# Kernel tuning notes

Hardware: AMD Instinct MI355X
Metric: run time of the kernel (lower is better)

Reference implementation:

```python
import jax, jax.numpy as jnp
import numpy as np


def setup_inputs() -> dict:
    key = jax.random.key(0)
    ks = jax.random.split(key, 8)
    B, S, V, E, H = 64, 128, 8000, 256, 512
    scale = 0.05
    return {
        "inputs": jax.random.randint(ks[0], (B, S), 0, V, dtype=jnp.int64),
        "embedding": jax.random.normal(ks[1], (V, E), dtype=jnp.float32) * scale,
        "W_ih": jax.random.normal(ks[2], (4 * H, E), dtype=jnp.float32) * scale,
        "W_hh": jax.random.normal(ks[3], (4 * H, H), dtype=jnp.float32) * scale,
        "b_ih": jax.random.normal(ks[4], (4 * H,), dtype=jnp.float32) * scale,
        "b_hh": jax.random.normal(ks[5], (4 * H,), dtype=jnp.float32) * scale,
        "W_cls": jax.random.normal(ks[6], (V, H), dtype=jnp.float32) * scale,
        "b_cls": jax.random.normal(ks[7], (V,), dtype=jnp.float32) * scale,
    }


def reference(inputs, embedding, W_ih, W_hh, b_ih, b_hh, W_cls, b_cls):
    B, S = inputs.shape
    H = W_hh.shape[1]
    x = embedding[inputs]  # (B, S, E)
    # batch the input-to-hidden GEMM across all timesteps
    x_gates = jnp.einsum('bse,ge->bsg', x, W_ih) + b_ih + b_hh  # (B, S, 4H)

    def step(carry, xg):
        h, c = carry
        gates = xg + h @ W_hh.T  # (B, 4H)
        i, f, g, o = jnp.split(gates, 4, axis=-1)  # PyTorch LSTMCell gate order
        i = jax.nn.sigmoid(i)
        f = jax.nn.sigmoid(f)
        g = jnp.tanh(g)
        o = jax.nn.sigmoid(o)
        c = f * c + i * g
        h = o * jnp.tanh(c)
        return (h, c), h

    h0 = jnp.zeros((B, H), dtype=x.dtype)
    c0 = jnp.zeros((B, H), dtype=x.dtype)
    _, hs = jax.lax.scan(step, (h0, c0), jnp.swapaxes(x_gates, 0, 1))  # hs: (S, B, H)
    hidden = jnp.swapaxes(hs, 0, 1)  # (B, S, H)
    logits = jnp.einsum('bsh,vh->bsv', hidden, W_cls) + b_cls  # (B, S, V)
    y = jnp.transpose(logits, (0, 2, 1))  # (B, V, S)
    return jax.nn.log_softmax(y, axis=1)
```

## Files before the change

### kernel.cpp

```cpp
#include <hip/hip_runtime.h>


using u16   = unsigned short;
using u32   = unsigned int;
using u16x8 = __attribute__((ext_vector_type(8))) u16;
using bf16x8 = __attribute__((ext_vector_type(8))) __bf16;
using f32x4 = __attribute__((ext_vector_type(4))) float;

#define NB   64
#define NS   128
#define NV   8000
#define NVP  8192
#define NE   256
#define NH   512
#define NG   2048
#define NBS  8192
#define OUT_BSTRIDE 1024000
#define XG_SSTRIDE  131072

__device__ inline u16 f2bf(float f) {
    unsigned x = __builtin_bit_cast(unsigned, f);
    unsigned r = (x + 0x7FFFu + ((x >> 16) & 1u)) >> 16;
    return (u16)r;
}

__device__ inline bf16x8 ld_frag(const u16* p) {
    u16x8 v = *(const u16x8*)p;
    return __builtin_bit_cast(bf16x8, v);
}

__device__ inline u32 load_llc(const u32* p) {
    u32 v;
    asm volatile("global_load_dword %0, %1, off sc0 sc1\n\t"
                 "s_waitcnt vmcnt(0)"
                 : "=v"(v) : "v"(p) : "memory");
    return v;
}
__device__ inline f32x4 load_llc16(const void* p) {
    f32x4 v;
    asm volatile("global_load_dwordx4 %0, %1, off sc0 sc1\n\t"
                 "s_waitcnt vmcnt(0)"
                 : "=v"(v) : "v"(p) : "memory");
    return v;
}
__device__ inline void store_llc(u32* p, u32 v) {
    asm volatile("global_store_dword %0, %1, off sc0 sc1"
                 :: "v"(p), "v"(v) : "memory");
}
__device__ inline void prefetch16(f32x4& d, const float* p) {
    asm volatile("global_load_dwordx4 %0, %1, off"
                 : "=v"(d) : "v"(p) : "memory");
}

__device__ inline void quad_transpose(float v[4], int p) {
    float tb[4];
    #pragma unroll
    for (int q2 = 0; q2 < 4; ++q2) tb[q2] = __shfl_xor(v[q2 ^ 2], 2);
    #pragma unroll
    for (int q2 = 0; q2 < 4; ++q2) v[q2] = (((q2 ^ p) & 2) ? tb[q2] : v[q2]);
    #pragma unroll
    for (int q2 = 0; q2 < 4; ++q2) tb[q2] = __shfl_xor(v[q2 ^ 1], 1);
    #pragma unroll
    for (int q2 = 0; q2 < 4; ++q2) v[q2] = (((q2 ^ p) & 1) ? tb[q2] : v[q2]);
}

__device__ inline float lstm_cell(const float v[4], float& c) {
    float i_ = 1.f / (1.f + __expf(-v[0]));
    float f_ = 1.f / (1.f + __expf(-v[1]));
    float e2 = __expf(2.f * v[2]);
    float g_ = 1.f - 2.f / (e2 + 1.f);
    float o_ = 1.f / (1.f + __expf(-v[3]));
    c = f_ * c + i_ * g_;
    float e2c = __expf(2.f * c);
    return o_ * (1.f - 2.f / (e2c + 1.f));
}

__global__ void cvt_bf16(const float* __restrict__ s, u16* __restrict__ d, int n8) {
    const float4* s4 = (const float4*)s;
    for (int i = blockIdx.x * blockDim.x + threadIdx.x; i < n8;
         i += gridDim.x * blockDim.x) {
        float4 a = s4[2 * i], b = s4[2 * i + 1];
        u16x8 o;
        o[0] = f2bf(a.x); o[1] = f2bf(a.y); o[2] = f2bf(a.z); o[3] = f2bf(a.w);
        o[4] = f2bf(b.x); o[5] = f2bf(b.y); o[6] = f2bf(b.z); o[7] = f2bf(b.w);
        ((u16x8*)d)[i] = o;
    }
}

__global__ __launch_bounds__(256) void k1_xgates(
    const u16* __restrict__ Wih, const u16* __restrict__ emb,
    const int* __restrict__ toks,
    const float* __restrict__ bih, const float* __restrict__ bhh,
    float* __restrict__ xg)
{
    __shared__ u16x8 Al8[512];
    __shared__ u16x8 Bl8[512];
    u16* Al = (u16*)Al8;
    u16* Bl = (u16*)Bl8;

    const int t = threadIdx.x;
    const int lane = t & 63, w = t >> 6;
    const int wm = w >> 1, wn = w & 1;
    const int gtile = blockIdx.y * 128, mtile = blockIdx.x * 128;

    const int r0 = t >> 2, r1 = r0 + 64, q = t & 3;
    const int m0 = mtile + r0, m1 = mtile + r1;
    const int tok0 = toks[(m0 & 63) * NS + (m0 >> 6)];
    const int tok1 = toks[(m1 & 63) * NS + (m1 >> 6)];

    f32x4 acc[4][4];
    for (int i = 0; i < 4; ++i)
        for (int j = 0; j < 4; ++j) acc[i][j] = {0.f, 0.f, 0.f, 0.f};

    const int kc8 = (lane >> 4) * 8;
    for (int kk = 0; kk < 8; ++kk) {
        const int k0 = kk * 32;
        *(u16x8*)&Al[t * 8]         = *(const u16x8*)&Wih[(gtile + r0) * NE + k0 + q * 8];
        *(u16x8*)&Al[(t + 256) * 8] = *(const u16x8*)&Wih[(gtile + r1) * NE + k0 + q * 8];
        *(u16x8*)&Bl[t * 8]         = *(const u16x8*)&emb[tok0 * NE + k0 + q * 8];
        *(u16x8*)&Bl[(t + 256) * 8] = *(const u16x8*)&emb[tok1 * NE + k0 + q * 8];
        __syncthreads();
        bf16x8 af[4], bf[4];
        #pragma unroll
        for (int i = 0; i < 4; ++i) {
            af[i] = ld_frag(&Al[(wm * 64 + i * 16 + (lane & 15)) * 32 + kc8]);
            bf[i] = ld_frag(&Bl[(wn * 64 + i * 16 + (lane & 15)) * 32 + kc8]);
        }
        #pragma unroll
        for (int fi = 0; fi < 4; ++fi)
            #pragma unroll
            for (int fj = 0; fj < 4; ++fj)
                acc[fi][fj] = __builtin_amdgcn_mfma_f32_16x16x32_bf16(
                    af[fi], bf[fj], acc[fi][fj], 0, 0, 0);
        __syncthreads();
    }

    #pragma unroll
    for (int fi = 0; fi < 4; ++fi) {
        const int g0 = gtile + wm * 64 + fi * 16 + ((lane >> 4) << 2);
        const float4 v1 = *(const float4*)&bih[g0];
        const float4 v2 = *(const float4*)&bhh[g0];
        float badd[4] = {v1.x + v2.x, v1.y + v2.y, v1.z + v2.z, v1.w + v2.w};
        #pragma unroll
        for (int fj = 0; fj < 4; ++fj) {
            const int m = mtile + wn * 64 + fj * 16 + (lane & 15);
            const int b = m & 63, s = m >> 6;
            float* dst = &xg[s * XG_SSTRIDE + b];
            #pragma unroll
            for (int r = 0; r < 4; ++r)
                dst[(g0 + r) * 64] = acc[fi][fj][r] + badd[r];
        }
    }
}

#define LSTM_NBLK 64

__global__ __launch_bounds__(512, 2) void k2_lstm(
    const u16* __restrict__ Whh,
    const float* __restrict__ xg,
    u16* __restrict__ hbuf,
    u16* __restrict__ hidden,
    u32* __restrict__ flags)
{
    __shared__ __align__(16) u16 hl[16 * 528];

    const int t = threadIdx.x, lane = t & 63, w = t >> 6;
    const int bg = blockIdx.x >> 3, ug = blockIdx.x & 7;
    const int j = lane & 15, kg = lane >> 4;
    const int kc8 = kg * 8;

    const int ubase = ug * 64 + w * 8;
    const int grow0 = (j & 3) * 512 + ubase + (j >> 2);
    const int grow1 = grow0 + 4;

    bf16x8 bw0[16], bw1[16];
    #pragma unroll
    for (int kk = 0; kk < 16; ++kk) {
        bw0[kk] = ld_frag(&Whh[grow0 * NH + kk * 32 + kc8]);
        bw1[kk] = ld_frag(&Whh[grow1 * NH + kk * 32 + kc8]);
    }
    #pragma unroll
    for (int kk = 0; kk < 16; ++kk) {
        f32x4 w0 = __builtin_bit_cast(f32x4, bw0[kk]);
        f32x4 w1 = __builtin_bit_cast(f32x4, bw1[kk]);
        asm volatile("" : "+v"(w0), "+v"(w1));
        bw0[kk] = __builtin_bit_cast(bf16x8, w0);
        bw1[kk] = __builtin_bit_cast(bf16x8, w1);
    }

    {
        u16x8 z = {0, 0, 0, 0, 0, 0, 0, 0};
        *(u16x8*)&hl[(8 + (t >> 6)) * 528 + (t & 63) * 8] = z;
    }

    const int srow = t >> 6, scol = (t & 63) * 8;
    const int soff = (bg * 8 + srow) * NH + scol;
    u16* hl_w = &hl[srow * 528 + scol];

    const int p  = lane & 3;
    const int q  = (lane >> 2) & 3;
    const int mb = kg * 4;
    const bool real = (kg < 2);
    const int bat = bg * 8 + mb + p;
    const int un0 = ubase + q;
    const bool sl = real && ((lane & 4) == 0);

    const int xo0 = grow0 * 64 + bg * 8 + mb;
    const int xo1 = grow1 * 64 + bg * 8 + mb;

    f32x4 xvA0 = {0,0,0,0}, xvA1 = {0,0,0,0};
    f32x4 xvB0 = {0,0,0,0}, xvB1 = {0,0,0,0};
    if (real) {
        xvA0 = *(const f32x4*)&xg[xo0];
        xvA1 = *(const f32x4*)&xg[xo1];
        xvB0 = *(const f32x4*)&xg[XG_SSTRIDE + xo0];
        xvB1 = *(const f32x4*)&xg[XG_SSTRIDE + xo1];
    }
    float cA = 0.f, cB = 0.f;

    auto body = [&](int step, f32x4& X0, f32x4& X1) {
        f32x4 a00 = {0,0,0,0}, a01 = {0,0,0,0};
        f32x4 a10 = {0,0,0,0}, a11 = {0,0,0,0};

        if (step > 0) {
            if (lane < 8) {
                const u32* fp = &flags[(bg * 8 + lane) * 32];
                while ((int)load_llc(fp) < step) __builtin_amdgcn_s_sleep(1);
            }
            f32x4 hv = load_llc16(&hbuf[(step & 1) * (NB * NH) + soff]);
            *(f32x4*)hl_w = hv;
            __syncthreads();

            #pragma unroll
            for (int kk = 0; kk < 16; ++kk) {
                bf16x8 av = *(const bf16x8*)&hl[j * 528 + kk * 32 + kc8];
                if (kk & 1) {
                    a01 = __builtin_amdgcn_mfma_f32_16x16x32_bf16(av, bw0[kk], a01, 0, 0, 0);
                    a11 = __builtin_amdgcn_mfma_f32_16x16x32_bf16(av, bw1[kk], a11, 0, 0, 0);
                } else {
                    a00 = __builtin_amdgcn_mfma_f32_16x16x32_bf16(av, bw0[kk], a00, 0, 0, 0);
                    a10 = __builtin_amdgcn_mfma_f32_16x16x32_bf16(av, bw1[kk], a10, 0, 0, 0);
                }
            }
        }

        float v0[4], v1[4];
        #pragma unroll
        for (int r = 0; r < 4; ++r) {
            v0[r] = a00[r] + a01[r] + X0[r];
            v1[r] = a10[r] + a11[r] + X1[r];
        }
        quad_transpose(v0, p);
        quad_transpose(v1, p);

        float h0 = lstm_cell(v0, cA);
        float h1 = lstm_cell(v1, cB);
        u32 hb0 = f2bf(h0), hb1 = f2bf(h1);
        u32 o0 = (u32)__shfl_xor((int)hb0, 4);
        u32 o1 = (u32)__shfl_xor((int)hb1, 4);
        u32 pr0 = hb0 | (o0 << 16);
        u32 pr1 = hb1 | (o1 << 16);

        if (step + 1 < NS && sl) {
            u32* hp = (u32*)&hbuf[((step + 1) & 1) * (NB * NH) + bat * NH + un0];
            store_llc(hp, pr0);
            store_llc(hp + 2, pr1);
        }
        if (step + 2 < NS && real) {
            const float* xb = &xg[(step + 2) * XG_SSTRIDE];
            prefetch16(X0, &xb[xo0]);
            prefetch16(X1, &xb[xo1]);
        }
        if (step + 2 < NS)
            asm volatile("s_waitcnt vmcnt(2) lgkmcnt(0)\n\ts_barrier" ::: "memory");
        else
            asm volatile("s_waitcnt vmcnt(0) lgkmcnt(0)\n\ts_barrier" ::: "memory");
        if (step + 1 < NS && t == 0)
            store_llc(&flags[blockIdx.x * 32], (u32)(step + 1));
        if (sl) {
            *(u32*)&hidden[(bat * NS + step) * NH + un0] = pr0;
            *(u32*)&hidden[(bat * NS + step) * NH + un0 + 4] = pr1;
        }
    };

    for (int s2 = 0; s2 < NS / 2; ++s2) {
        body(2 * s2,     xvA0, xvA1);
        body(2 * s2 + 1, xvB0, xvB1);
    }
}

__global__ __launch_bounds__(256) void k3_cls(
    const u16* __restrict__ Wc, const u16* __restrict__ hid,
    const float* __restrict__ bcls,
    float* __restrict__ out, float* __restrict__ lse)
{
    __shared__ u16x8 Al8[512];
    __shared__ u16x8 Bl8[512];
    __shared__ float red[2][128];
    u16* Al = (u16*)Al8;
    u16* Bl = (u16*)Bl8;

    const int t = threadIdx.x;
    const int lane = t & 63, w = t >> 6;
    const int wm = w >> 1, wn = w & 1;
    const int vtile = blockIdx.y * 128, mtile = blockIdx.x * 128;

    const int r0 = t >> 2, r1 = r0 + 64, q = t & 3;

    f32x4 acc[4][4];
    for (int i = 0; i < 4; ++i)
        for (int j2 = 0; j2 < 4; ++j2) acc[i][j2] = {0.f, 0.f, 0.f, 0.f};

    const int kc8 = (lane >> 4) * 8;
    for (int kk = 0; kk < 16; ++kk) {
        const int k0 = kk * 32;
        *(u16x8*)&Al[t * 8]         = *(const u16x8*)&Wc[(vtile + r0) * NH + k0 + q * 8];
        *(u16x8*)&Al[(t + 256) * 8] = *(const u16x8*)&Wc[(vtile + r1) * NH + k0 + q * 8];
        *(u16x8*)&Bl[t * 8]         = *(const u16x8*)&hid[(mtile + r0) * NH + k0 + q * 8];
        *(u16x8*)&Bl[(t + 256) * 8] = *(const u16x8*)&hid[(mtile + r1) * NH + k0 + q * 8];
        __syncthreads();
        bf16x8 af[4], bf[4];
        #pragma unroll
        for (int i = 0; i < 4; ++i) {
            af[i] = ld_frag(&Al[(wm * 64 + i * 16 + (lane & 15)) * 32 + kc8]);
            bf[i] = ld_frag(&Bl[(wn * 64 + i * 16 + (lane & 15)) * 32 + kc8]);
        }
        #pragma unroll
        for (int fi = 0; fi < 4; ++fi)
            #pragma unroll
            for (int fj = 0; fj < 4; ++fj)
                acc[fi][fj] = __builtin_amdgcn_mfma_f32_16x16x32_bf16(
                    af[fi], bf[fj], acc[fi][fj], 0, 0, 0);
        __syncthreads();
    }

    float lsum[4] = {0.f, 0.f, 0.f, 0.f};
    #pragma unroll
    for (int fi = 0; fi < 4; ++fi) {
        const int v0 = vtile + wm * 64 + fi * 16 + ((lane >> 4) << 2);
        const bool vok = (v0 < NV);
        float4 bc = {0.f, 0.f, 0.f, 0.f};
        if (vok) bc = *(const float4*)&bcls[v0];
        #pragma unroll
        for (int fj = 0; fj < 4; ++fj) {
            const int m = mtile + wn * 64 + fj * 16 + (lane & 15);
            const int b = m >> 7, s = m & 127;
            if (vok) {
                float* dst = &out[b * OUT_BSTRIDE + v0 * NS + s];
                float e = 0.f;
                #pragma unroll
                for (int r = 0; r < 4; ++r) {
                    float lg = acc[fi][fj][r] + (&bc.x)[r];
                    dst[r * NS] = lg;
                    e += __expf(lg);
                }
                lsum[fj] += e;
            }
        }
    }
    #pragma unroll
    for (int fj = 0; fj < 4; ++fj) {
        lsum[fj] += __shfl_xor(lsum[fj], 16);
        lsum[fj] += __shfl_xor(lsum[fj], 32);
    }
    if (lane < 16) {
        #pragma unroll
        for (int fj = 0; fj < 4; ++fj)
            red[wm][wn * 64 + fj * 16 + lane] = lsum[fj];
    }
    __syncthreads();
    if (t < 128) {
        const int m = mtile + t;
        atomicAdd(&lse[m], red[0][t] + red[1][t]);
    }
}

__global__ void k4_log(const float* __restrict__ lse, float* __restrict__ ll) {
    int i = blockIdx.x * 256 + threadIdx.x;
    if (i < NBS) ll[i] = logf(lse[i]);
}

__global__ void k5_norm(float* __restrict__ out, const float* __restrict__ ll) {
    const int total4 = NB * NV * NS / 4;
    float4* o4 = (float4*)out;
    for (int i = blockIdx.x * blockDim.x + threadIdx.x; i < total4;
         i += gridDim.x * blockDim.x) {
        const int i4 = i * 4;
        const int b = i4 / OUT_BSTRIDE;
        const int s = (i4 - b * OUT_BSTRIDE) & 127;
        float4 v = o4[i];
        const float4 l = *(const float4*)&ll[b * NS + s];
        v.x -= l.x; v.y -= l.y; v.z -= l.z; v.w -= l.w;
        o4[i] = v;
    }
}

extern "C" void kernel_launch(void* const* d_in, const int* in_sizes, int n_in,
                              void* d_out, int out_size, void* d_ws, size_t ws_size,
                              hipStream_t stream) {
    const int*   toks   = (const int*)d_in[0];
    const float* emb_f  = (const float*)d_in[1];
    const float* Wih_f  = (const float*)d_in[2];
    const float* Whh_f  = (const float*)d_in[3];
    const float* bih    = (const float*)d_in[4];
    const float* bhh    = (const float*)d_in[5];
    const float* Wcls_f = (const float*)d_in[6];
    const float* bcls   = (const float*)d_in[7];
    float* out = (float*)d_out;
    char*  ws  = (char*)d_ws;

    u32*   flags  = (u32*)(ws + 0);
    float* lse    = (float*)(ws + 8192);
    float* loglse = (float*)(ws + 40960);
    u16*   hbuf   = (u16*)(ws + 73728);
    u16*   embb   = (u16*)(ws + 204800);
    u16*   wihb   = (u16*)(ws + 4300800);
    u16*   whhb   = (u16*)(ws + 5349376);
    u16*   wclsb  = (u16*)(ws + 7446528);
    u16*   hidden = (u16*)(ws + 15835136);

    float* xg = out;

    hipMemsetAsync(ws, 0, 73728, stream);
    hipMemsetAsync((char*)wclsb + NV * NH * 2, 0, (NVP - NV) * NH * 2, stream);

    cvt_bf16<<<1024, 256, 0, stream>>>(emb_f,  embb,  NV * NE / 8);
    cvt_bf16<<<256,  256, 0, stream>>>(Wih_f,  wihb,  NG * NE / 8);
    cvt_bf16<<<512,  256, 0, stream>>>(Whh_f,  whhb,  NG * NH / 8);
    cvt_bf16<<<1024, 256, 0, stream>>>(Wcls_f, wclsb, NV * NH / 8);

    k1_xgates<<<dim3(64, 16), 256, 0, stream>>>(wihb, embb, toks, bih, bhh, xg);
    k2_lstm<<<LSTM_NBLK, 512, 0, stream>>>(whhb, xg, hbuf, hidden, flags);
    k3_cls<<<dim3(64, 64), 256, 0, stream>>>(wclsb, hidden, bcls, out, lse);
    k4_log<<<32, 256, 0, stream>>>(lse, loglse);
    k5_norm<<<2048, 256, 0, stream>>>(out, loglse);
}
```

Before: 684.3 us.

## Use per-wave flags and double-buffered LDS to drop the second block barrier per LSTM step

Replaces the per-block completion flag with one flag per wave, posted after that wave's hidden-state stores drain. Each thread now spins on a single producer-wave flag instead of eight lanes polling block flags. The shared h tile is double-buffered by step parity, so only one __syncthreads per step is needed and the trailing barrier is removed. The xg prefetch distance drops from two steps to one. The cost is more flag traffic and polling spread across all lanes, and the correctness of the flag indexing has to hold across blocks.

```diff
diff --git a/kernel.cpp b/kernel.cpp
--- a/kernel.cpp
+++ b/kernel.cpp
@@ -162,7 +162,7 @@
     u16* __restrict__ hidden,
     u32* __restrict__ flags)
 {
-    __shared__ __align__(16) u16 hl[16 * 528];
+    __shared__ __align__(16) u16 hl[2][16 * 528];
 
     const int t = threadIdx.x, lane = t & 63, w = t >> 6;
     const int bg = blockIdx.x >> 3, ug = blockIdx.x & 7;
@@ -190,12 +190,14 @@
 
     {
         u16x8 z = {0, 0, 0, 0, 0, 0, 0, 0};
-        *(u16x8*)&hl[(8 + (t >> 6)) * 528 + (t & 63) * 8] = z;
+        *(u16x8*)&hl[0][(8 + (t >> 6)) * 528 + (t & 63) * 8] = z;
+        *(u16x8*)&hl[1][(8 + (t >> 6)) * 528 + (t & 63) * 8] = z;
     }
 
     const int srow = t >> 6, scol = (t & 63) * 8;
     const int soff = (bg * 8 + srow) * NH + scol;
-    u16* hl_w = &hl[srow * 528 + scol];
+    const u32* myflag = flags + bg * 256 + (t & 63) * 4;
+    u32* ourflag = flags + bg * 256 + (ug * 8 + w) * 4;
 
     const int p  = lane & 3;
     const int q  = (lane >> 2) & 3;
@@ -208,32 +210,35 @@
     const int xo0 = grow0 * 64 + bg * 8 + mb;
     const int xo1 = grow1 * 64 + bg * 8 + mb;
 
-    f32x4 xvA0 = {0,0,0,0}, xvA1 = {0,0,0,0};
-    f32x4 xvB0 = {0,0,0,0}, xvB1 = {0,0,0,0};
+    f32x4 xv0 = {0,0,0,0}, xv1 = {0,0,0,0};
+    f32x4 xn0 = {0,0,0,0}, xn1 = {0,0,0,0};
     if (real) {
-        xvA0 = *(const f32x4*)&xg[xo0];
-        xvA1 = *(const f32x4*)&xg[xo1];
-        xvB0 = *(const f32x4*)&xg[XG_SSTRIDE + xo0];
-        xvB1 = *(const f32x4*)&xg[XG_SSTRIDE + xo1];
+        xv0 = *(const f32x4*)&xg[xo0];
+        xv1 = *(const f32x4*)&xg[xo1];
     }
     float cA = 0.f, cB = 0.f;
 
-    auto body = [&](int step, f32x4& X0, f32x4& X1) {
+    for (int step = 0; step < NS; ++step) {
+        const int par = step & 1;
+        if (step > 0) {
+            while ((int)load_llc(myflag) < step) __builtin_amdgcn_s_sleep(1);
+            f32x4 hv = load_llc16(&hbuf[par * (NB * NH) + soff]);
+            *(f32x4*)&hl[par][srow * 528 + scol] = hv;
+        }
+        __syncthreads();
+
+        if (step + 1 < NS && real) {
+            const float* xb = &xg[(step + 1) * XG_SSTRIDE];
+            prefetch16(xn0, &xb[xo0]);
+            prefetch16(xn1, &xb[xo1]);
+        }
+
         f32x4 a00 = {0,0,0,0}, a01 = {0,0,0,0};
         f32x4 a10 = {0,0,0,0}, a11 = {0,0,0,0};
-
         if (step > 0) {
-            if (lane < 8) {
-                const u32* fp = &flags[(bg * 8 + lane) * 32];
-                while ((int)load_llc(fp) < step) __builtin_amdgcn_s_sleep(1);
-            }
-            f32x4 hv = load_llc16(&hbuf[(step & 1) * (NB * NH) + soff]);
-            *(f32x4*)hl_w = hv;
-            __syncthreads();
-
             #pragma unroll
             for (int kk = 0; kk < 16; ++kk) {
-                bf16x8 av = *(const bf16x8*)&hl[j * 528 + kk * 32 + kc8];
+                bf16x8 av = *(const bf16x8*)&hl[par][j * 528 + kk * 32 + kc8];
                 if (kk & 1) {
                     a01 = __builtin_amdgcn_mfma_f32_16x16x32_bf16(av, bw0[kk], a01, 0, 0, 0);
                     a11 = __builtin_amdgcn_mfma_f32_16x16x32_bf16(av, bw1[kk], a11, 0, 0, 0);
@@ -247,8 +252,8 @@
         float v0[4], v1[4];
         #pragma unroll
         for (int r = 0; r < 4; ++r) {
-            v0[r] = a00[r] + a01[r] + X0[r];
-            v1[r] = a10[r] + a11[r] + X1[r];
+            v0[r] = a00[r] + a01[r] + xv0[r];
+            v1[r] = a10[r] + a11[r] + xv1[r];
         }
         quad_transpose(v0, p);
         quad_transpose(v1, p);
@@ -261,31 +266,21 @@
         u32 pr0 = hb0 | (o0 << 16);
         u32 pr1 = hb1 | (o1 << 16);
 
-        if (step + 1 < NS && sl) {
-            u32* hp = (u32*)&hbuf[((step + 1) & 1) * (NB * NH) + bat * NH + un0];
-            store_llc(hp, pr0);
-            store_llc(hp + 2, pr1);
-        }
-        if (step + 2 < NS && real) {
-            const float* xb = &xg[(step + 2) * XG_SSTRIDE];
-            prefetch16(X0, &xb[xo0]);
-            prefetch16(X1, &xb[xo1]);
-        }
-        if (step + 2 < NS)
-            asm volatile("s_waitcnt vmcnt(2) lgkmcnt(0)\n\ts_barrier" ::: "memory");
-        else
-            asm volatile("s_waitcnt vmcnt(0) lgkmcnt(0)\n\ts_barrier" ::: "memory");
-        if (step + 1 < NS && t == 0)
-            store_llc(&flags[blockIdx.x * 32], (u32)(step + 1));
+        if (step + 1 < NS) {
+            if (sl) {
+                u32* hp = (u32*)&hbuf[((step + 1) & 1) * (NB * NH) + bat * NH + un0];
+                store_llc(hp, pr0);
+                store_llc(hp + 2, pr1);
+            }
+            asm volatile("s_waitcnt vmcnt(0)" ::: "memory");
+            if (lane == 0)
+                store_llc(ourflag, (u32)(step + 1));
+        }
         if (sl) {
             *(u32*)&hidden[(bat * NS + step) * NH + un0] = pr0;
             *(u32*)&hidden[(bat * NS + step) * NH + un0 + 4] = pr1;
         }
-    };
-
-    for (int s2 = 0; s2 < NS / 2; ++s2) {
-        body(2 * s2,     xvA0, xvA1);
-        body(2 * s2 + 1, xvB0, xvB1);
+        xv0 = xn0; xv1 = xn1;
     }
 }
 
```

Result: slower. 944.2 us (+38.0%).
